# Performance work log

Hardware: AMD Instinct MI355X
Metric: run time of the kernel (lower is better)

Reference implementation:

```python
import jax, jax.numpy as jnp
import numpy as np


def setup_inputs() -> dict:
    key = jax.random.key(0)
    B, E, K = 1024, 1024, 64
    k0, k1, k2, k3, k4, k5 = jax.random.split(key, 6)
    s = 1.0 / np.sqrt(E)  # PyTorch GRU init bound
    c = jax.random.normal(k0, (B, E), dtype=jnp.float32)
    x = jax.random.normal(k1, (B, E, K), dtype=jnp.float32)
    W_ih = jax.random.uniform(k2, (3 * E, E), minval=-s, maxval=s, dtype=jnp.float32)
    W_hh = jax.random.uniform(k3, (3 * E, E), minval=-s, maxval=s, dtype=jnp.float32)
    b_ih = jax.random.uniform(k4, (3 * E,), minval=-s, maxval=s, dtype=jnp.float32)
    b_hh = jax.random.uniform(k5, (3 * E,), minval=-s, maxval=s, dtype=jnp.float32)
    return {"c": c, "x": x, "W_ih": W_ih, "W_hh": W_hh, "b_ih": b_ih, "b_hh": b_hh, "K": K}


def reference(c, x, W_ih, W_hh, b_ih, b_hh, K):
    # c: (B, E) initial hidden state; x: (B, E, T) teacher-forcing sequence.
    # Inputs actually consumed by the GRU: zeros at step 0, then x columns
    # [T-K .. T-2] at steps 1..K-1 (the torch slice at the last step is empty
    # and never used).
    B, E = c.shape
    T = x.shape[2]
    x_t = jnp.transpose(x, (2, 0, 1))  # (T, B, E)
    xs = jnp.concatenate(
        [jnp.zeros((1, B, E), dtype=x.dtype), x_t[T - K : T - 1]], axis=0
    )  # (K, B, E)

    def step(h, xk):
        gi = xk @ W_ih.T + b_ih  # (B, 3E)
        gh = h @ W_hh.T + b_hh   # (B, 3E)
        i_r, i_z, i_n = jnp.split(gi, 3, axis=-1)
        h_r, h_z, h_n = jnp.split(gh, 3, axis=-1)
        r = jax.nn.sigmoid(i_r + h_r)
        z = jax.nn.sigmoid(i_z + h_z)
        n = jnp.tanh(i_n + r * h_n)
        h_new = (1.0 - z) * n + z * h
        return h_new, h_new

    _, ys = jax.lax.scan(step, c, xs)  # ys: (K, B, E)
    y = jnp.transpose(ys, (1, 0, 2))   # (B, K, E) == torch.cat(y_out, dim=1)
    return jnp.transpose(y, (0, 2, 1))  # teacher-forcing transpose -> (B, E, K)
```

## Files before the change

### kernel.cpp

```cpp
#include <hip/hip_runtime.h>
#include <hip/hip_bf16.h>
#include <math.h>

typedef __bf16 bf16x8 __attribute__((ext_vector_type(8)));
typedef float f32x4 __attribute__((ext_vector_type(4)));
typedef unsigned short u16x8 __attribute__((ext_vector_type(8)));

#define VMW(N) asm volatile("s_waitcnt vmcnt(" #N ")" ::: "memory")
#define LGKM0  asm volatile("s_waitcnt lgkmcnt(0)" ::: "memory")
#define CFENCE asm volatile("" ::: "memory")

__device__ inline unsigned short f2b(float f) {
  union { float f; unsigned u; } v; v.f = f;
  unsigned u = v.u;
  return (unsigned short)((u + 0x7fffu + ((u >> 16) & 1u)) >> 16);
}
__device__ inline float b2f(unsigned short s) {
  union { unsigned u; float f; } v; v.u = ((unsigned)s) << 16;
  return v.f;
}
__device__ inline float sigm(float x) { return 1.f / (1.f + __expf(-x)); }
__device__ inline float tanh_f(float x) {
  float e = __expf(2.f * x);
  return 1.f - 2.f / (e + 1.f);
}
__device__ inline void gll16(const unsigned short* g, unsigned short* l) {
  __builtin_amdgcn_global_load_lds(
      (const __attribute__((address_space(1))) void*)g,
      (__attribute__((address_space(3))) void*)l, 16, 0, 0);
}
__device__ inline void gll16u(const unsigned short* g, unsigned short* l) {
  __builtin_amdgcn_global_load_lds(
      (const __attribute__((address_space(1))) void*)g,
      (__attribute__((address_space(3))) void*)l, 16, 0, 17);
}
__device__ inline void as64(unsigned short* p, unsigned long long v) {
  __hip_atomic_store((unsigned long long*)p, v, __ATOMIC_RELAXED,
                     __HIP_MEMORY_SCOPE_AGENT);
}

__global__ __launch_bounds__(256) void prep_kernel(
    const float* __restrict__ Wih, const float* __restrict__ Whh,
    const float* __restrict__ c, unsigned short* __restrict__ Wihb,
    unsigned short* __restrict__ Whhb, unsigned short* __restrict__ hbf,
    float* __restrict__ h32, long nW, long nH)
{
  long stride = (long)gridDim.x * blockDim.x;
  long t0 = (long)blockIdx.x * blockDim.x + threadIdx.x;
  for (long i = t0; i < nW; i += stride) {
    Wihb[i] = f2b(Wih[i]);
    Whhb[i] = f2b(Whh[i]);
  }
  for (long i = t0; i < nH; i += stride) {
    float v = c[i];
    h32[i] = v;
    hbf[i] = f2b(v);
  }
}

__global__ __launch_bounds__(256) void reorder_kernel(
    const unsigned short* __restrict__ Wihb, const unsigned short* __restrict__ Whhb,
    const float* __restrict__ bih, const float* __restrict__ bhh,
    unsigned short* __restrict__ Wihp, unsigned short* __restrict__ Whhp,
    float* __restrict__ bihp, float* __restrict__ bhhp, int E)
{
  int N3 = 3 * E;
  long total = (long)N3 * E;
  long stride = (long)gridDim.x * blockDim.x;
  long t0 = (long)blockIdx.x * blockDim.x + threadIdx.x;
  for (long i = t0; i < total; i += stride) {
    int rp = (int)(i / E);
    int col = (int)(i - (long)rp * E);
    int g6 = rp / 192, rem = rp - g6 * 192;
    int g = rem >> 6, elo = rem & 63;
    long src = ((long)g * E + g6 * 64 + elo) * E + col;
    Wihp[i] = Wihb[src];
    Whhp[i] = Whhb[src];
  }
  for (long i = t0; i < N3; i += stride) {
    int rp = (int)i;
    int g6 = rp / 192, rem = rp - g6 * 192;
    int g = rem >> 6, elo = rem & 63;
    bihp[i] = bih[(long)g * E + g6 * 64 + elo];
    bhhp[i] = bhh[(long)g * E + g6 * 64 + elo];
  }
}

__global__ __launch_bounds__(256) void transpose_x(
    const float* __restrict__ x, unsigned short* __restrict__ XS,
    int B, int E, int K)
{
  __shared__ float T[64][65];
  int e0 = blockIdx.x * 64;
  int b = blockIdx.y;
  int t = threadIdx.x;
  const float* xb = x + ((long)b * E + e0) * K;
#pragma unroll
  for (int i = 0; i < 4; ++i) {
    int cidx = i * 256 + t;
    int e = cidx >> 4;
    int f4 = cidx & 15;
    float4 v = *(const float4*)(xb + (long)e * K + f4 * 4);
    T[e][f4 * 4 + 0] = v.x;
    T[e][f4 * 4 + 1] = v.y;
    T[e][f4 * 4 + 2] = v.z;
    T[e][f4 * 4 + 3] = v.w;
  }
  __syncthreads();
#pragma unroll
  for (int i = 0; i < 16; ++i) {
    int cidx = i * 256 + t;
    int k = cidx >> 6;
    int e = cidx & 63;
    if (k < K - 1)
      XS[((long)(k + 1) * B + b) * E + e0 + e] = f2b(T[e][k]);
  }
}

__global__ __launch_bounds__(512, 1)
void gemm256(const unsigned short* __restrict__ A,
             const unsigned short* __restrict__ Bw,
             const float* __restrict__ bias,
             unsigned short* __restrict__ Cb,
             int M, int N, int K)
{
  __shared__ __align__(16) unsigned short sm[3 * 24576];

  int nwg = gridDim.x * gridDim.y;
  int wg = blockIdx.y * gridDim.x + blockIdx.x;
  if ((nwg & 7) == 0) { int ch = nwg >> 3; wg = (wg & 7) * ch + (wg >> 3); }
  int tx = wg % gridDim.x;
  int ty = wg / gridDim.x;

  const int tid = threadIdx.x;
  const int lane = tid & 63;
  const int wave = tid >> 6;
  const int wm = wave >> 2;
  const int wn = wave & 3;
  const int q = lane >> 4;
  const int l15 = lane & 15;

  const long a_base = (long)ty * 128 * K;
  const long b_base = (long)tx * 256 * K;

  long a_src[2]; int a_dst[2];
#pragma unroll
  for (int i = 0; i < 2; ++i) {
    int c = i * 512 + tid;
    int row = c >> 3;
    int g8 = (c & 7) ^ (row & 7);
    a_src[i] = a_base + (long)row * K + g8 * 8;
    a_dst[i] = c * 8;
  }
  long b_src[4]; int b_dst[4];
#pragma unroll
  for (int i = 0; i < 4; ++i) {
    int c = i * 512 + tid;
    int row = c >> 3;
    int g8 = (c & 7) ^ (row & 7);
    b_src[i] = b_base + (long)row * K + g8 * 8;
    b_dst[i] = c * 8;
  }

  int a_ro[4], b_ro[4];
#pragma unroll
  for (int mi = 0; mi < 4; ++mi) {
    int lr = wm * 64 + mi * 16 + l15;
    a_ro[mi] = lr * 64;
  }
#pragma unroll
  for (int ni = 0; ni < 4; ++ni) {
    int col = wn * 64 + ni * 16 + l15;
    b_ro[ni] = col * 64;
  }

  f32x4 acc[4][4] = {};

  const int NT = K >> 6;
#pragma unroll
  for (int t = 0; t < 2; ++t) {
    unsigned short* As = sm + t * 24576;
    unsigned short* Bs = As + 8192;
#pragma unroll
    for (int i = 0; i < 2; ++i) gll16(A + a_src[i] + t * 64, As + a_dst[i]);
#pragma unroll
    for (int i = 0; i < 4; ++i) gll16(Bw + b_src[i] + t * 64, Bs + b_dst[i]);
  }

  for (int kt = 0; kt < NT; ++kt) {
    if (kt >= NT - 2) VMW(0); else VMW(6);
    __builtin_amdgcn_s_barrier();
    CFENCE;
    const unsigned short* As = sm + (kt % 3) * 24576;
    const unsigned short* Bs = As + 8192;
    unsigned short* As2 = sm + ((kt + 2) % 3) * 24576;
    unsigned short* Bs2 = As2 + 8192;
    const bool st = (kt + 2 < NT);
    const int ko = (kt + 2) * 64;

    if (st) {
      gll16(A + a_src[0] + ko, As2 + a_dst[0]);
      gll16(A + a_src[1] + ko, As2 + a_dst[1]);
      gll16(Bw + b_src[0] + ko, Bs2 + b_dst[0]);
    }
    {
      const int c8 = q;
      bf16x8 af[4], bf_[4];
#pragma unroll
      for (int mi = 0; mi < 4; ++mi) {
        int lr = wm * 64 + mi * 16 + l15;
        af[mi] = *(const bf16x8*)&As[a_ro[mi] + ((c8 ^ (lr & 7)) << 3)];
      }
#pragma unroll
      for (int ni = 0; ni < 4; ++ni) {
        int col = wn * 64 + ni * 16 + l15;
        bf_[ni] = *(const bf16x8*)&Bs[b_ro[ni] + ((c8 ^ (col & 7)) << 3)];
      }
      __builtin_amdgcn_s_setprio(1);
#pragma unroll
      for (int mi = 0; mi < 4; ++mi)
#pragma unroll
        for (int ni = 0; ni < 4; ++ni)
          acc[mi][ni] = __builtin_amdgcn_mfma_f32_16x16x32_bf16(
              af[mi], bf_[ni], acc[mi][ni], 0, 0, 0);
      __builtin_amdgcn_s_setprio(0);
    }
    LGKM0;
    __builtin_amdgcn_s_barrier();
    CFENCE;
    if (st) {
      gll16(Bw + b_src[1] + ko, Bs2 + b_dst[1]);
      gll16(Bw + b_src[2] + ko, Bs2 + b_dst[2]);
      gll16(Bw + b_src[3] + ko, Bs2 + b_dst[3]);
    }
    {
      const int c8 = 4 + q;
      bf16x8 af[4], bf_[4];
#pragma unroll
      for (int mi = 0; mi < 4; ++mi) {
        int lr = wm * 64 + mi * 16 + l15;
        af[mi] = *(const bf16x8*)&As[a_ro[mi] + ((c8 ^ (lr & 7)) << 3)];
      }
#pragma unroll
      for (int ni = 0; ni < 4; ++ni) {
        int col = wn * 64 + ni * 16 + l15;
        bf_[ni] = *(const bf16x8*)&Bs[b_ro[ni] + ((c8 ^ (col & 7)) << 3)];
      }
      __builtin_amdgcn_s_setprio(1);
#pragma unroll
      for (int mi = 0; mi < 4; ++mi)
#pragma unroll
        for (int ni = 0; ni < 4; ++ni)
          acc[mi][ni] = __builtin_amdgcn_mfma_f32_16x16x32_bf16(
              af[mi], bf_[ni], acc[mi][ni], 0, 0, 0);
      __builtin_amdgcn_s_setprio(0);
    }
    LGKM0;
  }

  long crow0 = (long)ty * 128 + wm * 64;
  long ccol0 = (long)tx * 256 + wn * 64;
#pragma unroll
  for (int mi = 0; mi < 4; ++mi) {
#pragma unroll
    for (int ni = 0; ni < 4; ++ni) {
      long col = ccol0 + ni * 16 + l15;
      float bv = bias[col];
#pragma unroll
      for (int j = 0; j < 4; ++j) {
        long row = crow0 + mi * 16 + (q << 2) + j;
        Cb[row * N + col] = f2b(acc[mi][ni][j] + bv);
      }
    }
  }
}

#define BM 128
#define BN 128
#define BKS 64

template<int OUTBF>
__global__ __launch_bounds__(256)
void gemm_bt(const unsigned short* __restrict__ A,
             const unsigned short* __restrict__ Bw,
             const float* __restrict__ bias,
             float* __restrict__ Cf, unsigned short* __restrict__ Cb,
             int M, int N, int K)
{
  __shared__ __align__(16) unsigned short As[BM * BKS];
  __shared__ __align__(16) unsigned short Bs[BN * BKS];

  int nwg = gridDim.x * gridDim.y;
  int wg = blockIdx.y * gridDim.x + blockIdx.x;
  if ((nwg & 7) == 0) { int ch = nwg >> 3; wg = (wg & 7) * ch + (wg >> 3); }
  int tx = wg % gridDim.x;
  int ty = wg / gridDim.x;

  const int tid = threadIdx.x;
  const int lane = tid & 63;
  const int wave = tid >> 6;
  const int wr = wave >> 1, wc = wave & 1;

  f32x4 acc[4][4] = {};

  const long a_base = (long)ty * BM * K;
  const long b_base = (long)tx * BN * K;

  for (int kt = 0; kt < K; kt += BKS) {
    __syncthreads();
#pragma unroll
    for (int i = 0; i < 4; ++i) {
      int c = i * 256 + tid;
      int row = c >> 3, sc = c & 7;
      int gcol8 = sc ^ (row & 7);
      const unsigned short* ga = A + a_base + (long)row * K + kt + gcol8 * 8;
      const unsigned short* gb = Bw + b_base + (long)row * K + kt + gcol8 * 8;
      int cbase = (i * 256 + wave * 64) * 8;
      gll16(ga, &As[cbase]);
      gll16(gb, &Bs[cbase]);
    }
    __syncthreads();
#pragma unroll
    for (int kk = 0; kk < BKS; kk += 32) {
      int kidx = kk + ((lane >> 4) << 3);
      int c8 = kidx >> 3;
      bf16x8 af[4], bfv[4];
#pragma unroll
      for (int m = 0; m < 4; ++m) {
        int row = wr * 64 + m * 16 + (lane & 15);
        af[m] = *(const bf16x8*)&As[row * BKS + ((c8 ^ (row & 7)) << 3)];
      }
#pragma unroll
      for (int n = 0; n < 4; ++n) {
        int col = wc * 64 + n * 16 + (lane & 15);
        bfv[n] = *(const bf16x8*)&Bs[col * BKS + ((c8 ^ (col & 7)) << 3)];
      }
#pragma unroll
      for (int m = 0; m < 4; ++m)
#pragma unroll
        for (int n = 0; n < 4; ++n)
          acc[m][n] = __builtin_amdgcn_mfma_f32_16x16x32_bf16(
              af[m], bfv[n], acc[m][n], 0, 0, 0);
    }
  }

  long crow0 = (long)ty * BM + wr * 64;
  long ccol0 = (long)tx * BN + wc * 64;
#pragma unroll
  for (int m = 0; m < 4; ++m) {
#pragma unroll
    for (int n = 0; n < 4; ++n) {
      long col = ccol0 + n * 16 + (lane & 15);
      float bv = bias[col];
#pragma unroll
      for (int j = 0; j < 4; ++j) {
        long row = crow0 + m * 16 + ((lane >> 4) << 2) + j;
        float v = acc[m][n][j] + bv;
        if (OUTBF) Cb[row * N + col] = f2b(v);
        else       Cf[row * N + col] = v;
      }
    }
  }
}

__global__ __launch_bounds__(512, 1)
void gru_rec4(const unsigned short* __restrict__ GI,
              const unsigned short* __restrict__ Whp,
              const float* __restrict__ bhp,
              const unsigned short* __restrict__ h0,
              unsigned short* __restrict__ hbuf0,
              unsigned short* __restrict__ hbuf1,
              unsigned short* __restrict__ Y,
              unsigned int* __restrict__ bar,
              int B, int E, int K, int net)
{
  __shared__ __align__(16) unsigned char smem[156672];
  unsigned short* Ah  = (unsigned short*)smem;
  unsigned short* Bss = (unsigned short*)(smem + 49152);
  unsigned short* GIs = (unsigned short*)(smem + 122880);
  unsigned short* Ys  = (unsigned short*)(smem + 147456);
  float* Red = (float*)smem;

  const int N3 = 3 * E;
  const int e6 = blockIdx.x;
  const int bt = blockIdx.y;
  const int b0 = bt << 6;
  const int ec0 = e6 * 192;
  const int ecol0 = e6 << 6;
  const int tid = threadIdx.x;
  const int lane = tid & 63;
  const int w = tid >> 6;
  const int ew = w >> 1;
  const int kw = w & 1;
  const int q = lane >> 4;
  const int l15 = lane & 15;
  const int el = (ew << 4) + l15;
  const int c8 = (kw << 2) + q;
  const int axo = (c8 ^ (l15 & 7)) << 3;
  const int bxo = (c8 ^ (el & 7)) << 3;

  const int arow = tid >> 3;
  const int ag8 = (tid & 7) ^ (arow & 7);
  const long a_goff = (long)(b0 + arow) * E + ag8 * 8;
  const int a_dst = tid * 8;
  long b_goff[3]; int b_dst[3];
#pragma unroll
  for (int i = 0; i < 3; ++i) {
    int c = i * 512 + tid;
    int row = c >> 3;
    int g8 = (c & 7) ^ (row & 7);
    b_goff[i] = (long)(ec0 + row) * E + g8 * 8;
    b_dst[i] = c * 8;
  }
  long gi_off[3]; int gi_dst[3];
#pragma unroll
  for (int i = 0; i < 3; ++i) {
    int c = i * 512 + tid;
    int row = c / 24, cc = c - row * 24;
    gi_off[i] = (long)(b0 + row) * N3 + ec0 + cc * 8;
    gi_dst[i] = c * 8;
  }

  const float bh0 = bhp[ec0 + el];
  const float bh1 = bhp[ec0 + 64 + el];
  const float bh2 = bhp[ec0 + 128 + el];

  if (kw == 0) {
#pragma unroll
    for (int m = 0; m < 4; ++m)
#pragma unroll
      for (int j = 0; j < 4; ++j) {
        int row = m * 16 + q * 4 + j;
        Ys[row * 72 + el] = h0[(long)(b0 + row) * E + ecol0 + el];
      }
  }
  __syncthreads();

  for (int k = 0; k < K; ++k) {
    const unsigned short* hprev = (k & 1) ? hbuf1 : hbuf0;
    unsigned short* hnext = (k & 1) ? hbuf0 : hbuf1;
    const unsigned short* GIk = GI + (long)k * B * N3;

#pragma unroll
    for (int i = 0; i < 3; ++i) gll16(GIk + gi_off[i], GIs + gi_dst[i]);
#pragma unroll
    for (int t = 0; t < 5; ++t)
      gll16u(hprev + a_goff + t * 64, Ah + t * 4096 + a_dst);
#pragma unroll
    for (int t = 0; t < 2; ++t)
#pragma unroll
      for (int i = 0; i < 3; ++i)
        gll16(Whp + b_goff[i] + t * 64, Bss + t * 12288 + b_dst[i]);

    f32x4 acc[4][3];
#pragma unroll
    for (int m = 0; m < 4; ++m)
#pragma unroll
      for (int g = 0; g < 3; ++g)
        acc[m][g] = (f32x4){0.f, 0.f, 0.f, 0.f};

#pragma unroll
    for (int kt = 0; kt < 16; ++kt) {
      if (kt == 0)       VMW(3);
      else if (kt == 1)  VMW(4);
      else if (kt <= 11) VMW(5);
      else if (kt == 12) VMW(4);
      else if (kt == 15) VMW(0);
      else               VMW(3);
      LGKM0;
      __builtin_amdgcn_s_barrier();
      CFENCE;

      if (kt + 2 < 16) {
#pragma unroll
        for (int i = 0; i < 3; ++i)
          gll16(Whp + b_goff[i] + (kt + 2) * 64,
                Bss + ((kt + 2) % 3) * 12288 + b_dst[i]);
      }
      if (kt + 5 < 16)
        gll16u(hprev + a_goff + (kt + 5) * 64,
               Ah + ((kt + 5) % 6) * 4096 + a_dst);

      const unsigned short* Ab = Ah + (kt % 6) * 4096;
      const unsigned short* Bb = Bss + (kt % 3) * 12288;
      bf16x8 af[4], bfg[3];
#pragma unroll
      for (int m = 0; m < 4; ++m)
        af[m] = *(const bf16x8*)&Ab[(m * 16 + l15) * 64 + axo];
#pragma unroll
      for (int g = 0; g < 3; ++g)
        bfg[g] = *(const bf16x8*)&Bb[(g * 64 + el) * 64 + bxo];

      __builtin_amdgcn_s_setprio(1);
#pragma unroll
      for (int g = 0; g < 3; ++g)
#pragma unroll
        for (int m = 0; m < 4; ++m)
          acc[m][g] = __builtin_amdgcn_mfma_f32_16x16x32_bf16(
              af[m], bfg[g], acc[m][g], 0, 0, 0);
      __builtin_amdgcn_s_setprio(0);
    }

    __syncthreads();
    float* rp = &Red[((ew << 6) + lane) * 49];
    if (kw == 1) {
#pragma unroll
      for (int m = 0; m < 4; ++m)
#pragma unroll
        for (int g = 0; g < 3; ++g)
#pragma unroll
          for (int cc = 0; cc < 4; ++cc)
            rp[(m * 3 + g) * 4 + cc] = acc[m][g][cc];
    }
    __syncthreads();
    if (kw == 0) {
#pragma unroll
      for (int m = 0; m < 4; ++m) {
#pragma unroll
        for (int j = 0; j < 4; ++j) {
          int row = m * 16 + q * 4 + j;
          float ghr = acc[m][0][j] + rp[(m * 3 + 0) * 4 + j];
          float ghz = acc[m][1][j] + rp[(m * 3 + 1) * 4 + j];
          float ghn = acc[m][2][j] + rp[(m * 3 + 2) * 4 + j];
          float gr = b2f(GIs[row * 192 + el]);
          float gz = b2f(GIs[row * 192 + 64 + el]);
          float gn = b2f(GIs[row * 192 + 128 + el]);
          float hu = b2f(Ys[row * 72 + el]);
          float r = sigm(gr + ghr + bh0);
          float z = sigm(gz + ghz + bh1);
          float n = tanh_f(gn + r * (ghn + bh2));
          float hv = (1.f - z) * n + z * hu;
          Ys[row * 72 + el] = f2b(hv);
        }
      }
    }
    __syncthreads();
    {
      int row = tid >> 3, cc = tid & 7;
      u16x8 v = *(const u16x8*)&Ys[row * 72 + cc * 8];
      unsigned* pv = (unsigned*)&v;
      unsigned long long s0 = ((unsigned long long)pv[1] << 32) | pv[0];
      unsigned long long s1 = ((unsigned long long)pv[3] << 32) | pv[2];
      unsigned short* hp = hnext + (long)(b0 + row) * E + ecol0 + cc * 8;
      as64(hp, s0);
      as64(hp + 4, s1);
      *(u16x8*)(Y + ((long)k * B + b0 + row) * E + ecol0 + cc * 8) = v;
    }
    if (k + 1 < K) {
      __syncthreads();
      if (tid == 0) {
        __hip_atomic_fetch_add(&bar[bt * 64], 1u, __ATOMIC_RELAXED,
                               __HIP_MEMORY_SCOPE_AGENT);
        unsigned target = (unsigned)(k + 1) * (unsigned)net;
        while (__hip_atomic_load(&bar[bt * 64], __ATOMIC_RELAXED,
                                 __HIP_MEMORY_SCOPE_AGENT) < target)
          __builtin_amdgcn_s_sleep(1);
      }
      __syncthreads();
    }
  }
}

template<int YMODE>
__global__ __launch_bounds__(256)
void gru_pointwise(const unsigned short* __restrict__ GIk,
                   const float* __restrict__ gh,
                   float* __restrict__ h, unsigned short* __restrict__ hbf,
                   unsigned short* __restrict__ Yb,
                   float* __restrict__ out, int k, int B, int E, int K)
{
  long i4 = ((long)blockIdx.x * blockDim.x + threadIdx.x) * 4;
  if (i4 >= (long)B * E) return;
  long b = i4 / E;
  long e = i4 - b * E;
  long g0 = b * 3 * E + e;
  ushort4 ir = *(const ushort4*)(GIk + g0);
  ushort4 iz = *(const ushort4*)(GIk + g0 + E);
  ushort4 in4 = *(const ushort4*)(GIk + g0 + 2 * E);
  float4 hr = *(const float4*)(gh + g0);
  float4 hz = *(const float4*)(gh + g0 + E);
  float4 hn = *(const float4*)(gh + g0 + 2 * E);
  float4 hv = *(const float4*)(h + i4);

  float irf[4] = { b2f(ir.x), b2f(ir.y), b2f(ir.z), b2f(ir.w) };
  float izf[4] = { b2f(iz.x), b2f(iz.y), b2f(iz.z), b2f(iz.w) };
  float inf_[4] = { b2f(in4.x), b2f(in4.y), b2f(in4.z), b2f(in4.w) };
  float hrf[4] = { hr.x, hr.y, hr.z, hr.w };
  float hzf[4] = { hz.x, hz.y, hz.z, hz.w };
  float hnf[4] = { hn.x, hn.y, hn.z, hn.w };
  float hvf[4] = { hv.x, hv.y, hv.z, hv.w };
  float hnew[4];
#pragma unroll
  for (int j = 0; j < 4; ++j) {
    float r = sigm(irf[j] + hrf[j]);
    float z = sigm(izf[j] + hzf[j]);
    float n = tanh_f(inf_[j] + r * hnf[j]);
    hnew[j] = (1.f - z) * n + z * hvf[j];
  }
  *(float4*)(h + i4) = make_float4(hnew[0], hnew[1], hnew[2], hnew[3]);
  ushort4 hb = make_ushort4(f2b(hnew[0]), f2b(hnew[1]), f2b(hnew[2]), f2b(hnew[3]));
  *(ushort4*)(hbf + i4) = hb;
  if (YMODE == 1) {
    *(ushort4*)(Yb + ((long)k * B + b) * E + e) = hb;
  } else {
    float* o = out + (b * E + e) * K + k;
    o[0] = hnew[0]; o[K] = hnew[1]; o[2 * K] = hnew[2]; o[3 * K] = hnew[3];
  }
}

__global__ __launch_bounds__(256)
void transpose_y(const unsigned short* __restrict__ Yv, float* __restrict__ out,
                 int B, int E, int K)
{
  __shared__ float T[64][65];
  int e0 = blockIdx.x * 64;
  int b = blockIdx.y;
  int t = threadIdx.x;
#pragma unroll
  for (int i = 0; i < 4; ++i) {
    int c = i * 256 + t;
    int k = c >> 4, f4 = c & 15;
    long off = ((long)k * B + b) * E + e0 + f4 * 4;
    ushort4 v = *(const ushort4*)(Yv + off);
    T[k][f4 * 4 + 0] = b2f(v.x); T[k][f4 * 4 + 1] = b2f(v.y);
    T[k][f4 * 4 + 2] = b2f(v.z); T[k][f4 * 4 + 3] = b2f(v.w);
  }
  __syncthreads();
#pragma unroll
  for (int i = 0; i < 4; ++i) {
    int c = i * 256 + t;
    int e = c >> 4, f4k = c & 15;
    float4 w;
    w.x = T[f4k * 4 + 0][e];
    w.y = T[f4k * 4 + 1][e];
    w.z = T[f4k * 4 + 2][e];
    w.w = T[f4k * 4 + 3][e];
    *(float4*)(out + ((long)b * E + e0 + e) * K + f4k * 4) = w;
  }
}

extern "C" void kernel_launch(void* const* d_in, const int* in_sizes, int n_in,
                              void* d_out, int out_size, void* d_ws, size_t ws_size,
                              hipStream_t stream)
{
  const float* c   = (const float*)d_in[0];
  const float* x   = (const float*)d_in[1];
  const float* Wih = (const float*)d_in[2];
  const float* Whh = (const float*)d_in[3];
  const float* bih = (const float*)d_in[4];
  const float* bhh = (const float*)d_in[5];
  float* out = (float*)d_out;

  long BE = in_sizes[0];
  int E = (int)(sqrtf((float)(in_sizes[2] / 3)) + 0.5f);
  int B = (int)(BE / E);
  int K = (int)(in_sizes[1] / BE);
  int N3 = 3 * E;
  long M_GI = (long)K * B;

  char* w = (char*)d_ws;
  size_t used = 0;
  auto alloc = [&](size_t bytes) -> char* {
    char* p = w + used;
    used += (bytes + 255) & ~(size_t)255;
    return p;
  };
  unsigned short* Wihb  = (unsigned short*)alloc((size_t)N3 * E * 2);
  unsigned short* Whhb  = (unsigned short*)alloc((size_t)N3 * E * 2);
  unsigned short* hb0   = (unsigned short*)alloc((size_t)B * E * 2);
  float* h32            = (float*)alloc((size_t)B * E * 4);
  float* gh             = (float*)alloc((size_t)B * N3 * 4);
  unsigned short* GIstep= (unsigned short*)alloc((size_t)B * N3 * 2);
  unsigned short* XS    = (unsigned short*)alloc((size_t)K * B * E * 2);

  size_t rem = (ws_size > used) ? ws_size - used : 0;
  size_t szW   = (((size_t)N3 * E * 2) + 255) & ~(size_t)255;
  size_t szB3  = (((size_t)N3 * 4) + 255) & ~(size_t)255;
  size_t szHb1 = (((size_t)B * E * 2) + 255) & ~(size_t)255;
  size_t szGI  = (((size_t)K * B * N3 * 2) + 255) & ~(size_t)255;
  size_t szY   = (((size_t)K * B * E * 2) + 255) & ~(size_t)255;
  int nbt = B / 64, net = E / 64;
  size_t szBar = ((size_t)nbt * 64 * 4 + 255) & ~(size_t)255;

  bool canFused = (B == 1024) && (E == 1024) &&
                  (rem >= 2 * szW + 2 * szB3 + szHb1 + szGI + szY + szBar);

  long nW = (long)N3 * E;
  prep_kernel<<<dim3(2048), dim3(256), 0, stream>>>(Wih, Whh, c, Wihb, Whhb,
                                                    hb0, h32, nW, BE);
  hipMemsetAsync(XS, 0, (size_t)B * E * 2, stream);
  transpose_x<<<dim3(E / 64, B), dim3(256), 0, stream>>>(x, XS, B, E, K);

  if (canFused) {
    unsigned short* Wihp = (unsigned short*)alloc(szW);
    unsigned short* Whhp = (unsigned short*)alloc(szW);
    float* bihp          = (float*)alloc(szB3);
    float* bhhp          = (float*)alloc(szB3);
    unsigned short* hb1  = (unsigned short*)alloc(szHb1);
    unsigned short* GI   = (unsigned short*)alloc(szGI);
    unsigned short* Yb   = (unsigned short*)alloc(szY);
    unsigned int*   bar  = (unsigned int*)alloc(szBar);

    reorder_kernel<<<dim3(2048), dim3(256), 0, stream>>>(
        Wihb, Whhb, bih, bhh, Wihp, Whhp, bihp, bhhp, E);

    gemm256<<<dim3(N3 / 256, (int)(M_GI / 128)), dim3(512), 0, stream>>>(
        XS, Wihp, bihp, GI, (int)M_GI, N3, E);
    hipMemsetAsync(bar, 0, szBar, stream);

    const unsigned short* GIc = GI;
    const unsigned short* Whhc = Whhp;
    const float* bhhc = bhhp;
    const unsigned short* h0c = hb0;
    void* args[] = { (void*)&GIc, (void*)&Whhc, (void*)&bhhc, (void*)&h0c,
                     (void*)&hb0, (void*)&hb1, (void*)&Yb,
                     (void*)&bar, (void*)&B, (void*)&E, (void*)&K, (void*)&net };
    hipError_t ce = hipLaunchCooperativeKernel(
        (const void*)gru_rec4, dim3(net, nbt), dim3(512), args, 0, stream);
    if (ce != hipSuccess) {
      (void)hipGetLastError();
      gru_rec4<<<dim3(net, nbt), dim3(512), 0, stream>>>(
          GIc, Whhc, bhhc, h0c, hb0, hb1, Yb, bar, B, E, K, net);
    }
    transpose_y<<<dim3(E / 64, B), dim3(256), 0, stream>>>(Yb, out, B, E, K);
    return;
  }

  int haveY = rem >= szY;
  unsigned short* Yb = haveY ? (unsigned short*)alloc(szY) : nullptr;
  int pgrid = (int)((BE / 4 + 255) / 256);
  for (int k = 0; k < K; ++k) {
    gemm_bt<1><<<dim3(N3 / BN, B / BM), dim3(256), 0, stream>>>(
        XS + (size_t)k * B * E, Wihb, bih, nullptr, GIstep, B, N3, E);
    gemm_bt<0><<<dim3(N3 / BN, B / BM), dim3(256), 0, stream>>>(
        hb0, Whhb, bhh, gh, nullptr, B, N3, E);
    if (haveY)
      gru_pointwise<1><<<dim3(pgrid), dim3(256), 0, stream>>>(
          GIstep, gh, h32, hb0, Yb, out, k, B, E, K);
    else
      gru_pointwise<2><<<dim3(pgrid), dim3(256), 0, stream>>>(
          GIstep, gh, h32, hb0, nullptr, out, k, B, E, K);
  }
  if (haveY)
    transpose_y<<<dim3(E / 64, B), dim3(256), 0, stream>>>(Yb, out, B, E, K);
}
```

Baseline: 1.480 ms.

## Rotate K-loop start per block, reuse own h tile from LDS, prefetch weights before barrier

The recurrent GRU kernel now starts its K-dimension loop at a block-specific offset (rot = e6 & 15). The first A tile is then the block's own freshly computed hidden slice, which is copied from the Ys LDS buffer instead of being reloaded from global memory. The first two W_hh tiles for the next step are issued before the grid barrier so their latency overlaps the inter-block sync. Rotation also spreads concurrent global reads across different K chunks, at the cost of more complex waitcnt accounting.

```diff
diff --git a/kernel.cpp b/kernel.cpp
--- a/kernel.cpp
+++ b/kernel.cpp
@@ -364,7 +364,7 @@
 }
 
 __global__ __launch_bounds__(512, 1)
-void gru_rec4(const unsigned short* __restrict__ GI,
+void gru_rec6(const unsigned short* __restrict__ GI,
               const unsigned short* __restrict__ Whp,
               const float* __restrict__ bhp,
               const unsigned short* __restrict__ h0,
@@ -387,6 +387,7 @@
   const int b0 = bt << 6;
   const int ec0 = e6 * 192;
   const int ecol0 = e6 << 6;
+  const int rot = e6 & 15;
   const int tid = threadIdx.x;
   const int lane = tid & 63;
   const int w = tid >> 6;
@@ -436,21 +437,29 @@
   }
   __syncthreads();
 
+#pragma unroll
+  for (int i = 0; i < 3; ++i)
+    gll16(Whp + b_goff[i] + rot * 64, Bss + b_dst[i]);
+#pragma unroll
+  for (int i = 0; i < 3; ++i)
+    gll16(Whp + b_goff[i] + ((rot + 1) & 15) * 64, Bss + 12288 + b_dst[i]);
+
   for (int k = 0; k < K; ++k) {
     const unsigned short* hprev = (k & 1) ? hbuf1 : hbuf0;
     unsigned short* hnext = (k & 1) ? hbuf0 : hbuf1;
     const unsigned short* GIk = GI + (long)k * B * N3;
 
+    {
+      int row = tid >> 3;
+      int g8 = (tid & 7) ^ (row & 7);
+      u16x8 v = *(const u16x8*)&Ys[row * 72 + g8 * 8];
+      *(u16x8*)&Ah[a_dst] = v;
+    }
+#pragma unroll
+    for (int t = 1; t < 5; ++t)
+      gll16u(hprev + a_goff + ((rot + t) & 15) * 64, Ah + t * 4096 + a_dst);
 #pragma unroll
     for (int i = 0; i < 3; ++i) gll16(GIk + gi_off[i], GIs + gi_dst[i]);
-#pragma unroll
-    for (int t = 0; t < 5; ++t)
-      gll16u(hprev + a_goff + t * 64, Ah + t * 4096 + a_dst);
-#pragma unroll
-    for (int t = 0; t < 2; ++t)
-#pragma unroll
-      for (int i = 0; i < 3; ++i)
-        gll16(Whp + b_goff[i] + t * 64, Bss + t * 12288 + b_dst[i]);
 
     f32x4 acc[4][3];
 #pragma unroll
@@ -461,8 +470,7 @@
 
 #pragma unroll
     for (int kt = 0; kt < 16; ++kt) {
-      if (kt == 0)       VMW(3);
-      else if (kt == 1)  VMW(4);
+      if (kt <= 1)       VMW(10);
       else if (kt <= 11) VMW(5);
       else if (kt == 12) VMW(4);
       else if (kt == 15) VMW(0);
@@ -474,11 +482,11 @@
       if (kt + 2 < 16) {
 #pragma unroll
         for (int i = 0; i < 3; ++i)
-          gll16(Whp + b_goff[i] + (kt + 2) * 64,
+          gll16(Whp + b_goff[i] + ((rot + kt + 2) & 15) * 64,
                 Bss + ((kt + 2) % 3) * 12288 + b_dst[i]);
       }
       if (kt + 5 < 16)
-        gll16u(hprev + a_goff + (kt + 5) * 64,
+        gll16u(hprev + a_goff + ((rot + kt + 5) & 15) * 64,
                Ah + ((kt + 5) % 6) * 4096 + a_dst);
 
       const unsigned short* Ab = Ah + (kt % 6) * 4096;
@@ -547,7 +555,15 @@
       *(u16x8*)(Y + ((long)k * B + b0 + row) * E + ecol0 + cc * 8) = v;
     }
     if (k + 1 < K) {
-      __syncthreads();
+#pragma unroll
+      for (int i = 0; i < 3; ++i)
+        gll16(Whp + b_goff[i] + rot * 64, Bss + b_dst[i]);
+#pragma unroll
+      for (int i = 0; i < 3; ++i)
+        gll16(Whp + b_goff[i] + ((rot + 1) & 15) * 64, Bss + 12288 + b_dst[i]);
+      VMW(6);
+      __builtin_amdgcn_s_barrier();
+      CFENCE;
       if (tid == 0) {
         __hip_atomic_fetch_add(&bar[bt * 64], 1u, __ATOMIC_RELAXED,
                                __HIP_MEMORY_SCOPE_AGENT);
@@ -556,7 +572,8 @@
                                  __HIP_MEMORY_SCOPE_AGENT) < target)
           __builtin_amdgcn_s_sleep(1);
       }
-      __syncthreads();
+      __builtin_amdgcn_s_barrier();
+      CFENCE;
     }
   }
 }
@@ -716,10 +733,10 @@
                      (void*)&hb0, (void*)&hb1, (void*)&Yb,
                      (void*)&bar, (void*)&B, (void*)&E, (void*)&K, (void*)&net };
     hipError_t ce = hipLaunchCooperativeKernel(
-        (const void*)gru_rec4, dim3(net, nbt), dim3(512), args, 0, stream);
+        (const void*)gru_rec6, dim3(net, nbt), dim3(512), args, 0, stream);
     if (ce != hipSuccess) {
       (void)hipGetLastError();
-      gru_rec4<<<dim3(net, nbt), dim3(512), 0, stream>>>(
+      gru_rec6<<<dim3(net, nbt), dim3(512), 0, stream>>>(
           GIc, Whhc, bhhc, h0c, hb0, hb1, Yb, bar, B, E, K, net);
     }
     transpose_y<<<dim3(E / 64, B), dim3(256), 0, stream>>>(Yb, out, B, E, K);
```

Result: no change. 1.502 ms (+1.5%).

## Halve per-block GRU recurrence tile to run two 256-thread blocks per CU

Applied to the files above, without the earlier changes.

The cooperative recurrent kernel now gives each block 32 hidden columns instead of 64, using 256 threads and half the shared memory, and doubles the grid. Launch bounds allow two resident blocks per CU, and the A/B staging moves to a uniform 3-stage ring. The goal is more wave-level overlap of the recurrent GEMM and gate math on each CU. In exchange, every block re-reads the full hidden-state tile, so hidden-state traffic per step doubles, and the grid-wide barrier now spans twice as many blocks.

```diff
diff --git a/kernel.cpp b/kernel.cpp
--- a/kernel.cpp
+++ b/kernel.cpp
@@ -363,8 +363,8 @@
   }
 }
 
-__global__ __launch_bounds__(512, 1)
-void gru_rec4(const unsigned short* __restrict__ GI,
+__global__ __launch_bounds__(256, 2)
+void gru_rec7(const unsigned short* __restrict__ GI,
               const unsigned short* __restrict__ Whp,
               const float* __restrict__ bhp,
               const unsigned short* __restrict__ h0,
@@ -374,19 +374,21 @@
               unsigned int* __restrict__ bar,
               int B, int E, int K, int net)
 {
-  __shared__ __align__(16) unsigned char smem[156672];
+  __shared__ __align__(16) unsigned char smem[78848];
   unsigned short* Ah  = (unsigned short*)smem;
-  unsigned short* Bss = (unsigned short*)(smem + 49152);
-  unsigned short* GIs = (unsigned short*)(smem + 122880);
-  unsigned short* Ys  = (unsigned short*)(smem + 147456);
+  unsigned short* Bss = (unsigned short*)(smem + 24576);
+  unsigned short* GIs = (unsigned short*)(smem + 61440);
+  unsigned short* Ys  = (unsigned short*)(smem + 73728);
   float* Red = (float*)smem;
 
   const int N3 = 3 * E;
   const int e6 = blockIdx.x;
   const int bt = blockIdx.y;
   const int b0 = bt << 6;
-  const int ec0 = e6 * 192;
-  const int ecol0 = e6 << 6;
+  const int g6 = e6 >> 1;
+  const int half = e6 & 1;
+  const int prow0 = g6 * 192 + half * 32;
+  const int ecol0 = e6 << 5;
   const int tid = threadIdx.x;
   const int lane = tid & 63;
   const int w = tid >> 6;
@@ -399,31 +401,38 @@
   const int axo = (c8 ^ (l15 & 7)) << 3;
   const int bxo = (c8 ^ (el & 7)) << 3;
 
-  const int arow = tid >> 3;
-  const int ag8 = (tid & 7) ^ (arow & 7);
-  const long a_goff = (long)(b0 + arow) * E + ag8 * 8;
-  const int a_dst = tid * 8;
-  long b_goff[3]; int b_dst[3];
-#pragma unroll
-  for (int i = 0; i < 3; ++i) {
-    int c = i * 512 + tid;
+  long a_goff[2]; int a_dst[2];
+#pragma unroll
+  for (int i = 0; i < 2; ++i) {
+    int c = i * 256 + tid;
     int row = c >> 3;
     int g8 = (c & 7) ^ (row & 7);
-    b_goff[i] = (long)(ec0 + row) * E + g8 * 8;
+    a_goff[i] = (long)(b0 + row) * E + g8 * 8;
+    a_dst[i] = c * 8;
+  }
+  long b_goff[3]; int b_dst[3];
+#pragma unroll
+  for (int i = 0; i < 3; ++i) {
+    int c = i * 256 + tid;
+    int r = c >> 3;
+    int g8 = (c & 7) ^ (r & 7);
+    int g = r >> 5, rr = r & 31;
+    b_goff[i] = (long)(prow0 + g * 64 + rr) * E + g8 * 8;
     b_dst[i] = c * 8;
   }
   long gi_off[3]; int gi_dst[3];
 #pragma unroll
   for (int i = 0; i < 3; ++i) {
-    int c = i * 512 + tid;
-    int row = c / 24, cc = c - row * 24;
-    gi_off[i] = (long)(b0 + row) * N3 + ec0 + cc * 8;
-    gi_dst[i] = c * 8;
-  }
-
-  const float bh0 = bhp[ec0 + el];
-  const float bh1 = bhp[ec0 + 64 + el];
-  const float bh2 = bhp[ec0 + 128 + el];
+    int c = i * 256 + tid;
+    int row = c / 12, cc = c - row * 12;
+    int g = cc >> 2, j = cc & 3;
+    gi_off[i] = (long)(b0 + row) * N3 + prow0 + g * 64 + j * 8;
+    gi_dst[i] = row * 96 + g * 32 + j * 8;
+  }
+
+  const float bh0 = bhp[prow0 + el];
+  const float bh1 = bhp[prow0 + 64 + el];
+  const float bh2 = bhp[prow0 + 128 + el];
 
   if (kw == 0) {
 #pragma unroll
@@ -431,7 +440,7 @@
 #pragma unroll
       for (int j = 0; j < 4; ++j) {
         int row = m * 16 + q * 4 + j;
-        Ys[row * 72 + el] = h0[(long)(b0 + row) * E + ecol0 + el];
+        Ys[row * 40 + el] = h0[(long)(b0 + row) * E + ecol0 + el];
       }
   }
   __syncthreads();
@@ -444,13 +453,15 @@
 #pragma unroll
     for (int i = 0; i < 3; ++i) gll16(GIk + gi_off[i], GIs + gi_dst[i]);
 #pragma unroll
-    for (int t = 0; t < 5; ++t)
-      gll16u(hprev + a_goff + t * 64, Ah + t * 4096 + a_dst);
-#pragma unroll
-    for (int t = 0; t < 2; ++t)
-#pragma unroll
-      for (int i = 0; i < 3; ++i)
-        gll16(Whp + b_goff[i] + t * 64, Bss + t * 12288 + b_dst[i]);
+    for (int i = 0; i < 2; ++i) gll16u(hprev + a_goff[i], Ah + a_dst[i]);
+#pragma unroll
+    for (int i = 0; i < 3; ++i) gll16(Whp + b_goff[i], Bss + b_dst[i]);
+#pragma unroll
+    for (int i = 0; i < 2; ++i)
+      gll16u(hprev + a_goff[i] + 64, Ah + 4096 + a_dst[i]);
+#pragma unroll
+    for (int i = 0; i < 3; ++i)
+      gll16(Whp + b_goff[i] + 64, Bss + 6144 + b_dst[i]);
 
     f32x4 acc[4][3];
 #pragma unroll
@@ -461,12 +472,7 @@
 
 #pragma unroll
     for (int kt = 0; kt < 16; ++kt) {
-      if (kt == 0)       VMW(3);
-      else if (kt == 1)  VMW(4);
-      else if (kt <= 11) VMW(5);
-      else if (kt == 12) VMW(4);
-      else if (kt == 15) VMW(0);
-      else               VMW(3);
+      if (kt == 15) VMW(0); else VMW(5);
       LGKM0;
       __builtin_amdgcn_s_barrier();
       CFENCE;
@@ -475,21 +481,22 @@
 #pragma unroll
         for (int i = 0; i < 3; ++i)
           gll16(Whp + b_goff[i] + (kt + 2) * 64,
-                Bss + ((kt + 2) % 3) * 12288 + b_dst[i]);
-      }
-      if (kt + 5 < 16)
-        gll16u(hprev + a_goff + (kt + 5) * 64,
-               Ah + ((kt + 5) % 6) * 4096 + a_dst);
-
-      const unsigned short* Ab = Ah + (kt % 6) * 4096;
-      const unsigned short* Bb = Bss + (kt % 3) * 12288;
+                Bss + ((kt + 2) % 3) * 6144 + b_dst[i]);
+#pragma unroll
+        for (int i = 0; i < 2; ++i)
+          gll16u(hprev + a_goff[i] + (kt + 2) * 64,
+                 Ah + ((kt + 2) % 3) * 4096 + a_dst[i]);
+      }
+
+      const unsigned short* Ab = Ah + (kt % 3) * 4096;
+      const unsigned short* Bb = Bss + (kt % 3) * 6144;
       bf16x8 af[4], bfg[3];
 #pragma unroll
       for (int m = 0; m < 4; ++m)
         af[m] = *(const bf16x8*)&Ab[(m * 16 + l15) * 64 + axo];
 #pragma unroll
       for (int g = 0; g < 3; ++g)
-        bfg[g] = *(const bf16x8*)&Bb[(g * 64 + el) * 64 + bxo];
+        bfg[g] = *(const bf16x8*)&Bb[(g * 32 + el) * 64 + bxo];
 
       __builtin_amdgcn_s_setprio(1);
 #pragma unroll
@@ -522,22 +529,22 @@
           float ghr = acc[m][0][j] + rp[(m * 3 + 0) * 4 + j];
           float ghz = acc[m][1][j] + rp[(m * 3 + 1) * 4 + j];
           float ghn = acc[m][2][j] + rp[(m * 3 + 2) * 4 + j];
-          float gr = b2f(GIs[row * 192 + el]);
-          float gz = b2f(GIs[row * 192 + 64 + el]);
-          float gn = b2f(GIs[row * 192 + 128 + el]);
-          float hu = b2f(Ys[row * 72 + el]);
+          float gr = b2f(GIs[row * 96 + el]);
+          float gz = b2f(GIs[row * 96 + 32 + el]);
+          float gn = b2f(GIs[row * 96 + 64 + el]);
+          float hu = b2f(Ys[row * 40 + el]);
           float r = sigm(gr + ghr + bh0);
           float z = sigm(gz + ghz + bh1);
           float n = tanh_f(gn + r * (ghn + bh2));
           float hv = (1.f - z) * n + z * hu;
-          Ys[row * 72 + el] = f2b(hv);
+          Ys[row * 40 + el] = f2b(hv);
         }
       }
     }
     __syncthreads();
     {
-      int row = tid >> 3, cc = tid & 7;
-      u16x8 v = *(const u16x8*)&Ys[row * 72 + cc * 8];
+      int row = tid >> 2, cc = tid & 3;
+      u16x8 v = *(const u16x8*)&Ys[row * 40 + cc * 8];
       unsigned* pv = (unsigned*)&v;
       unsigned long long s0 = ((unsigned long long)pv[1] << 32) | pv[0];
       unsigned long long s1 = ((unsigned long long)pv[3] << 32) | pv[2];
@@ -679,7 +686,7 @@
   size_t szHb1 = (((size_t)B * E * 2) + 255) & ~(size_t)255;
   size_t szGI  = (((size_t)K * B * N3 * 2) + 255) & ~(size_t)255;
   size_t szY   = (((size_t)K * B * E * 2) + 255) & ~(size_t)255;
-  int nbt = B / 64, net = E / 64;
+  int nbt = B / 64, net32 = E / 32;
   size_t szBar = ((size_t)nbt * 64 * 4 + 255) & ~(size_t)255;
 
   bool canFused = (B == 1024) && (E == 1024) &&
@@ -714,13 +721,13 @@
     const unsigned short* h0c = hb0;
     void* args[] = { (void*)&GIc, (void*)&Whhc, (void*)&bhhc, (void*)&h0c,
                      (void*)&hb0, (void*)&hb1, (void*)&Yb,
-                     (void*)&bar, (void*)&B, (void*)&E, (void*)&K, (void*)&net };
+                     (void*)&bar, (void*)&B, (void*)&E, (void*)&K, (void*)&net32 };
     hipError_t ce = hipLaunchCooperativeKernel(
-        (const void*)gru_rec4, dim3(net, nbt), dim3(512), args, 0, stream);
+        (const void*)gru_rec7, dim3(net32, nbt), dim3(256), args, 0, stream);
     if (ce != hipSuccess) {
       (void)hipGetLastError();
-      gru_rec4<<<dim3(net, nbt), dim3(512), 0, stream>>>(
-          GIc, Whhc, bhhc, h0c, hb0, hb1, Yb, bar, B, E, K, net);
+      gru_rec7<<<dim3(net32, nbt), dim3(256), 0, stream>>>(
+          GIc, Whhc, bhhc, h0c, hb0, hb1, Yb, bar, B, E, K, net32);
     }
     transpose_y<<<dim3(E / 64, B), dim3(256), 0, stream>>>(Yb, out, B, E, K);
     return;
```

Measured after the change: 1.516 ms. +2.5%, slower.

## Load recurrent GEMM operands directly into registers instead of staging through LDS

Applied to the files above, without the earlier changes.

The recurrent GRU kernel stops staging h and W_hh tiles in shared memory. Each wave now loads its MFMA fragments straight from global memory into registers, with a software pipeline in registers: h is read three k-tiles ahead with agent-scope atomic 64-bit loads, and W_hh two tiles ahead. This removes the per-k-tile block barriers and the LDS round trips, and the smaller LDS footprint allows launch bounds of two blocks per CU. The cost is more register pressure, uncoalesced per-lane global reads of the weights that rely on cache reuse, and many small atomic loads for h.

```diff
diff --git a/kernel.cpp b/kernel.cpp
--- a/kernel.cpp
+++ b/kernel.cpp
@@ -29,14 +29,18 @@
       (const __attribute__((address_space(1))) void*)g,
       (__attribute__((address_space(3))) void*)l, 16, 0, 0);
 }
-__device__ inline void gll16u(const unsigned short* g, unsigned short* l) {
-  __builtin_amdgcn_global_load_lds(
-      (const __attribute__((address_space(1))) void*)g,
-      (__attribute__((address_space(3))) void*)l, 16, 0, 17);
+__device__ inline unsigned long long al64(const unsigned short* p) {
+  return __hip_atomic_load((const unsigned long long*)p, __ATOMIC_RELAXED,
+                           __HIP_MEMORY_SCOPE_AGENT);
 }
 __device__ inline void as64(unsigned short* p, unsigned long long v) {
   __hip_atomic_store((unsigned long long*)p, v, __ATOMIC_RELAXED,
                      __HIP_MEMORY_SCOPE_AGENT);
+}
+__device__ inline bf16x8 pack16(unsigned long long a, unsigned long long b) {
+  union { unsigned long long u[2]; bf16x8 v; } c;
+  c.u[0] = a; c.u[1] = b;
+  return c.v;
 }
 
 __global__ __launch_bounds__(256) void prep_kernel(
@@ -363,8 +367,8 @@
   }
 }
 
-__global__ __launch_bounds__(512, 1)
-void gru_rec4(const unsigned short* __restrict__ GI,
+__global__ __launch_bounds__(512, 2)
+void gru_rec8(const unsigned short* __restrict__ GI,
               const unsigned short* __restrict__ Whp,
               const float* __restrict__ bhp,
               const unsigned short* __restrict__ h0,
@@ -374,12 +378,9 @@
               unsigned int* __restrict__ bar,
               int B, int E, int K, int net)
 {
-  __shared__ __align__(16) unsigned char smem[156672];
-  unsigned short* Ah  = (unsigned short*)smem;
-  unsigned short* Bss = (unsigned short*)(smem + 49152);
-  unsigned short* GIs = (unsigned short*)(smem + 122880);
-  unsigned short* Ys  = (unsigned short*)(smem + 147456);
-  float* Red = (float*)smem;
+  __shared__ __align__(16) unsigned short GIs[12288];
+  __shared__ __align__(16) unsigned short Ys[64 * 72];
+  __shared__ float Red[4 * 64 * 49];
 
   const int N3 = 3 * E;
   const int e6 = blockIdx.x;
@@ -395,23 +396,7 @@
   const int q = lane >> 4;
   const int l15 = lane & 15;
   const int el = (ew << 4) + l15;
-  const int c8 = (kw << 2) + q;
-  const int axo = (c8 ^ (l15 & 7)) << 3;
-  const int bxo = (c8 ^ (el & 7)) << 3;
-
-  const int arow = tid >> 3;
-  const int ag8 = (tid & 7) ^ (arow & 7);
-  const long a_goff = (long)(b0 + arow) * E + ag8 * 8;
-  const int a_dst = tid * 8;
-  long b_goff[3]; int b_dst[3];
-#pragma unroll
-  for (int i = 0; i < 3; ++i) {
-    int c = i * 512 + tid;
-    int row = c >> 3;
-    int g8 = (c & 7) ^ (row & 7);
-    b_goff[i] = (long)(ec0 + row) * E + g8 * 8;
-    b_dst[i] = c * 8;
-  }
+
   long gi_off[3]; int gi_dst[3];
 #pragma unroll
   for (int i = 0; i < 3; ++i) {
@@ -421,6 +406,15 @@
     gi_dst[i] = c * 8;
   }
 
+  long a_rp[4];
+#pragma unroll
+  for (int m = 0; m < 4; ++m)
+    a_rp[m] = (long)(b0 + m * 16 + l15) * E + kw * 32 + q * 8;
+  const unsigned short* wp[3];
+#pragma unroll
+  for (int g = 0; g < 3; ++g)
+    wp[g] = Whp + (long)(ec0 + g * 64 + el) * E + kw * 32 + q * 8;
+
   const float bh0 = bhp[ec0 + el];
   const float bh1 = bhp[ec0 + 64 + el];
   const float bh2 = bhp[ec0 + 128 + el];
@@ -443,14 +437,22 @@
 
 #pragma unroll
     for (int i = 0; i < 3; ++i) gll16(GIk + gi_off[i], GIs + gi_dst[i]);
-#pragma unroll
-    for (int t = 0; t < 5; ++t)
-      gll16u(hprev + a_goff + t * 64, Ah + t * 4096 + a_dst);
+
+    unsigned long long Au[3][4][2];
+    bf16x8 Bv[2][3];
+#pragma unroll
+    for (int t = 0; t < 3; ++t)
+#pragma unroll
+      for (int m = 0; m < 4; ++m) {
+        const unsigned short* p = hprev + a_rp[m] + t * 64;
+        Au[t][m][0] = al64(p);
+        Au[t][m][1] = al64(p + 4);
+      }
 #pragma unroll
     for (int t = 0; t < 2; ++t)
 #pragma unroll
-      for (int i = 0; i < 3; ++i)
-        gll16(Whp + b_goff[i] + t * 64, Bss + t * 12288 + b_dst[i]);
+      for (int g = 0; g < 3; ++g)
+        Bv[t][g] = *(const bf16x8*)(wp[g] + t * 64);
 
     f32x4 acc[4][3];
 #pragma unroll
@@ -461,43 +463,35 @@
 
 #pragma unroll
     for (int kt = 0; kt < 16; ++kt) {
-      if (kt == 0)       VMW(3);
-      else if (kt == 1)  VMW(4);
-      else if (kt <= 11) VMW(5);
-      else if (kt == 12) VMW(4);
-      else if (kt == 15) VMW(0);
-      else               VMW(3);
-      LGKM0;
-      __builtin_amdgcn_s_barrier();
-      CFENCE;
-
+      const int sa = kt % 3;
+      const int sb = kt & 1;
+      bf16x8 af[4];
+#pragma unroll
+      for (int m = 0; m < 4; ++m)
+        af[m] = pack16(Au[sa][m][0], Au[sa][m][1]);
+      bf16x8 bg0 = Bv[sb][0], bg1 = Bv[sb][1], bg2 = Bv[sb][2];
+
+      if (kt + 3 < 16) {
+#pragma unroll
+        for (int m = 0; m < 4; ++m) {
+          const unsigned short* p = hprev + a_rp[m] + (kt + 3) * 64;
+          Au[sa][m][0] = al64(p);
+          Au[sa][m][1] = al64(p + 4);
+        }
+      }
       if (kt + 2 < 16) {
 #pragma unroll
-        for (int i = 0; i < 3; ++i)
-          gll16(Whp + b_goff[i] + (kt + 2) * 64,
-                Bss + ((kt + 2) % 3) * 12288 + b_dst[i]);
-      }
-      if (kt + 5 < 16)
-        gll16u(hprev + a_goff + (kt + 5) * 64,
-               Ah + ((kt + 5) % 6) * 4096 + a_dst);
-
-      const unsigned short* Ab = Ah + (kt % 6) * 4096;
-      const unsigned short* Bb = Bss + (kt % 3) * 12288;
-      bf16x8 af[4], bfg[3];
-#pragma unroll
-      for (int m = 0; m < 4; ++m)
-        af[m] = *(const bf16x8*)&Ab[(m * 16 + l15) * 64 + axo];
-#pragma unroll
-      for (int g = 0; g < 3; ++g)
-        bfg[g] = *(const bf16x8*)&Bb[(g * 64 + el) * 64 + bxo];
+        for (int g = 0; g < 3; ++g)
+          Bv[sb][g] = *(const bf16x8*)(wp[g] + (kt + 2) * 64);
+      }
 
       __builtin_amdgcn_s_setprio(1);
 #pragma unroll
-      for (int g = 0; g < 3; ++g)
-#pragma unroll
-        for (int m = 0; m < 4; ++m)
-          acc[m][g] = __builtin_amdgcn_mfma_f32_16x16x32_bf16(
-              af[m], bfg[g], acc[m][g], 0, 0, 0);
+      for (int m = 0; m < 4; ++m) {
+        acc[m][0] = __builtin_amdgcn_mfma_f32_16x16x32_bf16(af[m], bg0, acc[m][0], 0, 0, 0);
+        acc[m][1] = __builtin_amdgcn_mfma_f32_16x16x32_bf16(af[m], bg1, acc[m][1], 0, 0, 0);
+        acc[m][2] = __builtin_amdgcn_mfma_f32_16x16x32_bf16(af[m], bg2, acc[m][2], 0, 0, 0);
+      }
       __builtin_amdgcn_s_setprio(0);
     }
 
@@ -716,10 +710,10 @@
                      (void*)&hb0, (void*)&hb1, (void*)&Yb,
                      (void*)&bar, (void*)&B, (void*)&E, (void*)&K, (void*)&net };
     hipError_t ce = hipLaunchCooperativeKernel(
-        (const void*)gru_rec4, dim3(net, nbt), dim3(512), args, 0, stream);
+        (const void*)gru_rec8, dim3(net, nbt), dim3(512), args, 0, stream);
     if (ce != hipSuccess) {
       (void)hipGetLastError();
-      gru_rec4<<<dim3(net, nbt), dim3(512), 0, stream>>>(
+      gru_rec8<<<dim3(net, nbt), dim3(512), 0, stream>>>(
           GIc, Whhc, bhhc, h0c, hb0, hb1, Yb, bar, B, E, K, net);
     }
     transpose_y<<<dim3(E / 64, B), dim3(256), 0, stream>>>(Yb, out, B, E, K);
```

Result: slower. 3.561 ms (+140.6%).
